# Kernel tuning notes

Hardware: AMD Instinct MI355X
Metric: run time of the kernel (lower is better)

Reference implementation:

```python
import jax, jax.numpy as jnp
from jax import lax
import numpy as np

N, L, C, G, K = 8, 4096, 256, 8, 3
GC = C // G
DILATION = 1
OFFSET_SCALE = 1.0
LN_EPS = 1e-6


def setup_inputs() -> dict:
    key = jax.random.key(0)
    ks = jax.random.split(key, 14)
    s = lambda k, shp, sc: jax.random.normal(k, shp, jnp.float32) * sc
    return {
        "x": jax.random.normal(ks[0], (N, L, C), jnp.float32),
        "W_in": s(ks[1], (C, C), (1.0 / C) ** 0.5),      # input_proj (in,out)
        "b_in": jnp.zeros((C,), jnp.float32),
        "conv_w": s(ks[2], (C, 1, K), 0.2),              # depthwise conv (O, I/g, K)
        "conv_b": jnp.zeros((C,), jnp.float32),
        "ln_g": jnp.ones((C,), jnp.float32),
        "ln_b": jnp.zeros((C,), jnp.float32),
        "W_off": s(ks[3], (C, G * K), 0.02),             # offset_linear
        "b_off": s(ks[4], (G * K,), 0.02),
        "W_mask": s(ks[5], (C, G * K), 0.02),            # mask_linear
        "b_mask": s(ks[6], (G * K,), 0.02),
        "W_out": s(ks[7], (C, C), (1.0 / C) ** 0.5),     # output_proj
        "b_out": jnp.zeros((C,), jnp.float32),
    }


def _dcnv3_1d(x, W_in, b_in, conv_w, conv_b, ln_g, ln_b,
              W_off, b_off, W_mask, b_mask, W_out, b_out):
    # x: (N, L, C)
    x_proj = x @ W_in + b_in                                     # (N,L,C)

    # depthwise conv -> LayerNorm(C) -> GELU  (the offset/mask feature branch)
    xc = x.transpose(0, 2, 1)                                    # (N,C,L)
    pad = (K - 1) // 2
    y = lax.conv_general_dilated(
        xc, conv_w, window_strides=(1,), padding=[(pad, pad)],
        dimension_numbers=("NCH", "OIH", "NCH"), feature_group_count=C)
    y = y + conv_b[None, :, None]
    y = y.transpose(0, 2, 1)                                     # (N,L,C)
    mu = y.mean(-1, keepdims=True)
    var = ((y - mu) ** 2).mean(-1, keepdims=True)
    y = (y - mu) * lax.rsqrt(var + LN_EPS) * ln_g + ln_b
    x_feat = jax.nn.gelu(y, approximate=False)                   # torch GELU = exact erf

    offset = (x_feat @ W_off + b_off).reshape(N, L, G, K)
    mask = jax.nn.softmax((x_feat @ W_mask + b_mask).reshape(N, L, G, K), axis=-1)

    # sampling locations (grid_sample with align_corners=True unnormalizes back to loc)
    ref_p = jnp.arange(L, dtype=jnp.float32)                     # (L,)
    lo = float(-((K - 1) // 2))
    hi = float((K - 1) // 2)
    dil_grid = jnp.linspace(lo, hi, K) * DILATION                # (K,)
    loc = ref_p[None, :, None, None] + dil_grid[None, None, None, :] \
          + offset * OFFSET_SCALE                                # (N,L,G,K)
    loc = jnp.remainder(loc, L)                                  # in [0, L)

    # bilinear sample along L with zero padding (matches F.grid_sample, H=1)
    f0 = jnp.floor(loc)
    w1 = loc - f0
    w0 = 1.0 - w1
    i0 = jnp.clip(f0.astype(jnp.int32), 0, L - 1)
    i1 = i0 + 1
    valid1 = (i1 < L)
    i1c = jnp.where(valid1, i1, 0)

    x_g = x_proj.reshape(N, L, G, GC)                            # (N,L,G,gc)
    nidx = jnp.arange(N)[:, None, None, None]
    gidx = jnp.arange(G)[None, None, :, None]
    v0 = x_g[nidx, i0, gidx]                                     # (N,L,G,K,gc)
    v1 = x_g[nidx, i1c, gidx] * valid1[..., None].astype(x_g.dtype)
    sampled = w0[..., None] * v0 + w1[..., None] * v1            # (N,L,G,K,gc)

    out = (sampled * mask[..., None]).sum(axis=3)                # (N,L,G,gc)
    out = out.reshape(N, L, C)
    return out @ W_out + b_out


def reference(x, W_in, b_in, conv_w, conv_b, ln_g, ln_b,
              W_off, b_off, W_mask, b_mask, W_out, b_out):
    return _dcnv3_1d(x, W_in, b_in, conv_w, conv_b, ln_g, ln_b,
                     W_off, b_off, W_mask, b_mask, W_out, b_out)
```

## Files before the change

### kernel.cpp

```cpp
#include <hip/hip_runtime.h>
#include <math.h>

constexpr int LL = 4096;
constexpr int CC = 256;
constexpr int MM = 32768;

typedef unsigned int u32;
typedef unsigned short u16;
typedef __attribute__((ext_vector_type(8))) short bf16x8;
typedef __attribute__((ext_vector_type(4))) float f32x4;

__device__ __forceinline__ u16 f2b(float f) {
    u32 u = __float_as_uint(f);
    u32 r = (u + 0x7fffu + ((u >> 16) & 1u)) >> 16;
    return (u16)r;
}
__device__ __forceinline__ u32 pack2(float a, float b) {
    return (u32)f2b(a) | ((u32)f2b(b) << 16);
}

__device__ __forceinline__ void gl_lds16(const u16* g, u16* l) {
    __builtin_amdgcn_global_load_lds(
        (const __attribute__((address_space(1))) unsigned int*)g,
        (__attribute__((address_space(3))) unsigned int*)l, 16, 0, 0);
}

__global__ __launch_bounds__(256) void conv_prep(
    const float* __restrict__ x, const float* __restrict__ cw,
    const float* __restrict__ cbias, const float* __restrict__ lng,
    const float* __restrict__ lnb, u16* __restrict__ xf,
    const float* __restrict__ W_in, const float* __restrict__ W_out,
    const float* __restrict__ W_off, const float* __restrict__ W_mask,
    u16* __restrict__ Wt_in, u16* __restrict__ Wt_out, u16* __restrict__ Wcomb)
{
    const int bid = blockIdx.x;
    const int t = threadIdx.x;
    if (bid >= 4096) {
        const int b = bid - 4096;
        if (b < 256) {
            Wt_in[b * 256 + t]  = f2b(W_in[t * 256 + b]);
            Wt_out[b * 256 + t] = f2b(W_out[t * 256 + b]);
        } else {
            const int j = b - 256;
            const float v = (j < 24) ? W_off[t * 24 + j] : W_mask[t * 24 + (j - 24)];
            Wcomb[j * 256 + t] = f2b(v);
        }
        return;
    }

    const int wave = t >> 6;
    const int lane = t & 63;
    const int nl0 = (bid << 3) + wave * 2;
    const int l0 = nl0 & (LL - 1);
    const int c0 = lane << 2;
    const size_t base = (size_t)nl0 * CC + c0;

    const float4 zero = make_float4(0.f, 0.f, 0.f, 0.f);
    float4 xm = (l0 > 0) ? *(const float4*)&x[base - CC] : zero;
    float4 xa = *(const float4*)&x[base];
    float4 xb = *(const float4*)&x[base + CC];
    float4 xp = (l0 < LL - 2) ? *(const float4*)&x[base + 2 * CC] : zero;

    const float cw0[4] = {cw[(c0+0)*3+0], cw[(c0+1)*3+0], cw[(c0+2)*3+0], cw[(c0+3)*3+0]};
    const float cw1[4] = {cw[(c0+0)*3+1], cw[(c0+1)*3+1], cw[(c0+2)*3+1], cw[(c0+3)*3+1]};
    const float cw2[4] = {cw[(c0+0)*3+2], cw[(c0+1)*3+2], cw[(c0+2)*3+2], cw[(c0+3)*3+2]};
    const float cb4[4] = {cbias[c0+0], cbias[c0+1], cbias[c0+2], cbias[c0+3]};
    const float lg4[4] = {lng[c0+0], lng[c0+1], lng[c0+2], lng[c0+3]};
    const float lb4[4] = {lnb[c0+0], lnb[c0+1], lnb[c0+2], lnb[c0+3]};

    const float pA[4] = {xm.x, xm.y, xm.z, xm.w};
    const float cA[4] = {xa.x, xa.y, xa.z, xa.w};
    const float nA[4] = {xb.x, xb.y, xb.z, xb.w};
    const float nB[4] = {xp.x, xp.y, xp.z, xp.w};

    float yA[4], yB[4];
    float sA = 0.f, qA = 0.f, sB = 0.f, qB = 0.f;
#pragma unroll
    for (int j = 0; j < 4; ++j) {
        float vA = fmaf(pA[j], cw0[j], fmaf(cA[j], cw1[j], fmaf(nA[j], cw2[j], cb4[j])));
        float vB = fmaf(cA[j], cw0[j], fmaf(nA[j], cw1[j], fmaf(nB[j], cw2[j], cb4[j])));
        yA[j] = vA; sA += vA; qA += vA * vA;
        yB[j] = vB; sB += vB; qB += vB * vB;
    }
#pragma unroll
    for (int off = 32; off > 0; off >>= 1) {
        sA += __shfl_xor(sA, off);
        qA += __shfl_xor(qA, off);
        sB += __shfl_xor(sB, off);
        qB += __shfl_xor(qB, off);
    }
    const float muA = sA * (1.f / CC), muB = sB * (1.f / CC);
    const float rsA = rsqrtf(qA * (1.f / CC) - muA * muA + 1e-6f);
    const float rsB = rsqrtf(qB * (1.f / CC) - muB * muB + 1e-6f);

    ushort4 oA, oB;
    float vA[4], vB[4];
#pragma unroll
    for (int j = 0; j < 4; ++j) {
        const float tA = (yA[j] - muA) * rsA * lg4[j] + lb4[j];
        const float tB = (yB[j] - muB) * rsB * lg4[j] + lb4[j];
        vA[j] = 0.5f * tA * (1.f + erff(tA * 0.70710678118654752f));
        vB[j] = 0.5f * tB * (1.f + erff(tB * 0.70710678118654752f));
    }
    oA.x = f2b(vA[0]); oA.y = f2b(vA[1]); oA.z = f2b(vA[2]); oA.w = f2b(vA[3]);
    oB.x = f2b(vB[0]); oB.y = f2b(vB[1]); oB.z = f2b(vB[2]); oB.w = f2b(vB[3]);
    *(ushort4*)&xf[base] = oA;
    *(ushort4*)&xf[base + CC] = oB;
}

__global__ __launch_bounds__(256) void proj_soft(
    const u16* __restrict__ xfeatb, const u16* __restrict__ Wcomb,
    const float* __restrict__ boff, const float* __restrict__ bmask,
    uint2* __restrict__ rec)
{
    __shared__ float logit[64 * 50];

    const int t = threadIdx.x;
    const int w = t >> 6, lane = t & 63;
    const int lr = lane & 15, lk8 = (lane >> 4) * 8;
    const int r0 = (lane >> 4) * 4;
    const int blk = blockIdx.x;
    const size_t row0 = (size_t)blk * 64;

    f32x4 pacc[3];
#pragma unroll
    for (int ct = 0; ct < 3; ++ct) pacc[ct] = f32x4{0.f, 0.f, 0.f, 0.f};
    const u16* fbase = xfeatb + (row0 + w * 16 + lr) * 256;
#pragma unroll
    for (int ks = 0; ks < 8; ++ks) {
        const int ke = ks * 32 + lk8;
        bf16x8 a = *(const bf16x8*)(fbase + ke);
#pragma unroll
        for (int ct = 0; ct < 3; ++ct) {
            bf16x8 bfr = *(const bf16x8*)(Wcomb + (size_t)(ct * 16 + lr) * 256 + ke);
            pacc[ct] = __builtin_amdgcn_mfma_f32_16x16x32_bf16(a, bfr, pacc[ct], 0, 0, 0);
        }
    }
#pragma unroll
    for (int ct = 0; ct < 3; ++ct) {
        const int j = ct * 16 + lr;
        const float bj = (j < 24) ? boff[j] : bmask[j - 24];
#pragma unroll
        for (int r4 = 0; r4 < 4; ++r4)
            logit[(w * 16 + r0 + r4) * 50 + j] = pacc[ct][r4] + bj;
    }
    __syncthreads();

#pragma unroll
    for (int pi = 0; pi < 2; ++pi) {
        const int pp = pi * 256 + t;
        const int rw = pp >> 3, g = pp & 7;
        const float* lp = &logit[rw * 50];
        const float m0v = lp[24 + g * 3 + 0];
        const float m1v = lp[24 + g * 3 + 1];
        const float m2v = lp[24 + g * 3 + 2];
        const float mx = fmaxf(m0v, fmaxf(m1v, m2v));
        const float e0 = expf(m0v - mx), e1 = expf(m1v - mx), e2 = expf(m2v - mx);
        const float inv = 1.f / (e0 + e1 + e2);
        const float msk[3] = {e0 * inv, e1 * inv, e2 * inv};
        const float lf = (float)((blk & 63) * 64 + rw);
        uint2* rbase = rec + row0 * 24 + pp * 3;
#pragma unroll
        for (int k = 0; k < 3; ++k) {
            const float loc = lf + (float)(k - 1) + lp[g * 3 + k];
            float r = fmodf(loc, (float)LL);
            if (r < 0.f) r += (float)LL;
            const float f0 = floorf(r);
            int i0 = (int)f0;
            i0 = i0 < 0 ? 0 : (i0 > LL - 1 ? LL - 1 : i0);
            const int i1 = i0 + 1;
            const float w1 = r - f0;
            const bool valid = (i1 < LL);
            union { u32 uw; _Float16 h[2]; } uh;
            uh.h[0] = (_Float16)(msk[k] * (1.f - w1));
            uh.h[1] = (_Float16)(valid ? msk[k] * w1 : 0.f);
            const u32 ij = (u32)i0 | ((u32)(valid ? i1 : 0) << 16);
            rbase[k] = make_uint2(uh.uw, ij);
        }
    }
}

__global__ __launch_bounds__(256, 2) void gemm1(
    const float* __restrict__ x, const u16* __restrict__ Wt_in,
    const float* __restrict__ b_in, u16* __restrict__ xprojb)
{
    __shared__ u16 As[2][128 * 32];
    __shared__ u16 Bs[2][128 * 32];

    const int t = threadIdx.x;
    const int w = t >> 6, lane = t & 63;
    const int lr = lane & 15, lk = lane >> 4;
    const int wm = w >> 1, wn = w & 1;

    const int d = blockIdx.x;
    const int m_t = (d & 7) * 32 + (d >> 4);
    const int n_t = (d >> 3) & 1;
    const int m0 = m_t * 128, n0 = n_t * 128;

    const int srow = lane >> 2;
    const int scol = (lane & 3) * 8;
    const int arow = t >> 1;
    const int akh = (t & 1) * 16;

    f32x4 acc[4][4];
#pragma unroll
    for (int i = 0; i < 4; ++i)
#pragma unroll
        for (int j = 0; j < 4; ++j) acc[i][j] = f32x4{0.f, 0.f, 0.f, 0.f};

    auto STAGE_B = [&](int buf, int kt) {
        const int k0 = kt * 32;
#pragma unroll
        for (int j = 0; j < 2; ++j) {
            const int rr = (w * 2 + j) * 16 + srow;
            gl_lds16(Wt_in + ((size_t)(n0 + rr) << 8) + k0 + scol,
                     &Bs[buf][0] + (w * 2 + j) * 512);
        }
    };
    const float* Abase = x + (size_t)(m0 + arow) * 256 + akh;

    {
        float4 f0 = *(const float4*)(Abase);
        float4 f1 = *(const float4*)(Abase + 4);
        float4 f2 = *(const float4*)(Abase + 8);
        float4 f3 = *(const float4*)(Abase + 12);
        STAGE_B(0, 0);
        u16* dst = &As[0][arow * 32 + akh];
        ((u32*)dst)[0] = pack2(f0.x, f0.y); ((u32*)dst)[1] = pack2(f0.z, f0.w);
        ((u32*)dst)[2] = pack2(f1.x, f1.y); ((u32*)dst)[3] = pack2(f1.z, f1.w);
        ((u32*)dst)[4] = pack2(f2.x, f2.y); ((u32*)dst)[5] = pack2(f2.z, f2.w);
        ((u32*)dst)[6] = pack2(f3.x, f3.y); ((u32*)dst)[7] = pack2(f3.z, f3.w);
    }

#pragma unroll
    for (int kt = 0; kt < 8; ++kt) {
        const int cur = kt & 1;
        __syncthreads();
        float4 f0, f1, f2, f3;
        if (kt < 7) {
            const float* ap = Abase + (kt + 1) * 32;
            f0 = *(const float4*)(ap);
            f1 = *(const float4*)(ap + 4);
            f2 = *(const float4*)(ap + 8);
            f3 = *(const float4*)(ap + 12);
            STAGE_B(cur ^ 1, kt + 1);
        }
        bf16x8 af[4], bfr[4];
#pragma unroll
        for (int mt = 0; mt < 4; ++mt)
            af[mt] = *(const bf16x8*)&As[cur][(wm * 64 + mt * 16 + lr) * 32 + lk * 8];
#pragma unroll
        for (int nt = 0; nt < 4; ++nt)
            bfr[nt] = *(const bf16x8*)&Bs[cur][(wn * 64 + nt * 16 + lr) * 32 + lk * 8];
#pragma unroll
        for (int mt = 0; mt < 4; ++mt)
#pragma unroll
            for (int nt = 0; nt < 4; ++nt)
                acc[mt][nt] = __builtin_amdgcn_mfma_f32_16x16x32_bf16(
                    af[mt], bfr[nt], acc[mt][nt], 0, 0, 0);
        if (kt < 7) {
            u16* dst = &As[cur ^ 1][arow * 32 + akh];
            ((u32*)dst)[0] = pack2(f0.x, f0.y); ((u32*)dst)[1] = pack2(f0.z, f0.w);
            ((u32*)dst)[2] = pack2(f1.x, f1.y); ((u32*)dst)[3] = pack2(f1.z, f1.w);
            ((u32*)dst)[4] = pack2(f2.x, f2.y); ((u32*)dst)[5] = pack2(f2.z, f2.w);
            ((u32*)dst)[6] = pack2(f3.x, f3.y); ((u32*)dst)[7] = pack2(f3.z, f3.w);
        }
    }

    const int r0 = lk * 4;
#pragma unroll
    for (int nt = 0; nt < 4; ++nt) {
        const int cn = n0 + wn * 64 + nt * 16 + lr;
        const float bv = b_in[cn];
#pragma unroll
        for (int mt = 0; mt < 4; ++mt)
#pragma unroll
            for (int r4 = 0; r4 < 4; ++r4)
                xprojb[(size_t)(m0 + wm * 64 + mt * 16 + r0 + r4) * 256 + cn] =
                    f2b(acc[mt][nt][r4] + bv);
    }
}

__global__ __launch_bounds__(256, 4) void gather_gemm(
    const uint2* __restrict__ rec, const u16* __restrict__ xprojb,
    const u16* __restrict__ Wt_out, const float* __restrict__ b_out,
    float* __restrict__ out)
{
    __shared__ __align__(16) char s_mem[16384];
    __shared__ uint2 s_pack[768];

    const int t = threadIdx.x;
    const int w = t >> 6, lane = t & 63;
    const int lr = lane & 15, lk8 = (lane >> 4) * 8;
    const int r0 = (lane >> 4) * 4;
    const int blk = blockIdx.x;
    const size_t row0 = (size_t)blk * 32;

    {
        const uint2* rb = rec + row0 * 24;
#pragma unroll
        for (int e = 0; e < 3; ++e) s_pack[t * 3 + e] = rb[t * 3 + e];
    }
    __syncthreads();

    {
        const int ig = t >> 5, tc = t & 31;
        const int c0 = tc * 8, g4 = tc >> 2;
        const u16* xpn = xprojb + (size_t)(blk >> 7) * LL * 256;
        const int ibeg = ig * 4;
#pragma unroll
        for (int i = ibeg; i < ibeg + 4; ++i) {
            const int bidx = (i * 8 + g4) * 3;
            float v[8] = {0.f, 0.f, 0.f, 0.f, 0.f, 0.f, 0.f, 0.f};
#pragma unroll
            for (int k = 0; k < 3; ++k) {
                const uint2 pk = s_pack[bidx + k];
                union { u32 uw; _Float16 h[2]; } uh; uh.uw = pk.x;
                const float wa = (float)uh.h[0], wb = (float)uh.h[1];
                const int i0 = (int)(pk.y & 0xffffu), i1 = (int)(pk.y >> 16);
                uint4 ua = *(const uint4*)(xpn + (size_t)i0 * 256 + c0);
                uint4 ub = *(const uint4*)(xpn + (size_t)i1 * 256 + c0);
                const u32 au[4] = {ua.x, ua.y, ua.z, ua.w};
                const u32 bu[4] = {ub.x, ub.y, ub.z, ub.w};
#pragma unroll
                for (int j = 0; j < 4; ++j) {
                    v[2 * j]     = fmaf(wa, __uint_as_float(au[j] << 16),
                                   fmaf(wb, __uint_as_float(bu[j] << 16), v[2 * j]));
                    v[2 * j + 1] = fmaf(wa, __uint_as_float(au[j] & 0xffff0000u),
                                   fmaf(wb, __uint_as_float(bu[j] & 0xffff0000u), v[2 * j + 1]));
                }
            }
            uint4 wd;
            wd.x = pack2(v[0], v[1]); wd.y = pack2(v[2], v[3]);
            wd.z = pack2(v[4], v[5]); wd.w = pack2(v[6], v[7]);
            const int addr = (i * 512 + tc * 16) ^ ((i & 7) << 4);
            *(uint4*)(s_mem + addr) = wd;
        }
    }
    __syncthreads();

    f32x4 acc[2][4];
#pragma unroll
    for (int i = 0; i < 2; ++i)
#pragma unroll
        for (int j = 0; j < 4; ++j) acc[i][j] = f32x4{0.f, 0.f, 0.f, 0.f};

    const u16* Bw = Wt_out + (size_t)(w * 64) * 256;
#pragma unroll
    for (int ks = 0; ks < 8; ++ks) {
        bf16x8 af[2], bfr[4];
#pragma unroll
        for (int mt = 0; mt < 2; ++mt) {
            const int rm = mt * 16 + lr;
            const int addr = (rm * 512 + ks * 64 + lk8 * 2) ^ ((rm & 7) << 4);
            af[mt] = *(const bf16x8*)(s_mem + addr);
        }
        const int ke = ks * 32 + lk8;
#pragma unroll
        for (int nt = 0; nt < 4; ++nt)
            bfr[nt] = *(const bf16x8*)(Bw + (size_t)(nt * 16 + lr) * 256 + ke);
#pragma unroll
        for (int mt = 0; mt < 2; ++mt)
#pragma unroll
            for (int nt = 0; nt < 4; ++nt)
                acc[mt][nt] = __builtin_amdgcn_mfma_f32_16x16x32_bf16(
                    af[mt], bfr[nt], acc[mt][nt], 0, 0, 0);
    }
#pragma unroll
    for (int nt = 0; nt < 4; ++nt) {
        const int cn = w * 64 + nt * 16 + lr;
        const float bv = b_out[cn];
#pragma unroll
        for (int mt = 0; mt < 2; ++mt)
#pragma unroll
            for (int r4 = 0; r4 < 4; ++r4)
                out[(row0 + mt * 16 + r0 + r4) * 256 + cn] = acc[mt][nt][r4] + bv;
    }
}

extern "C" void kernel_launch(void* const* d_in, const int* in_sizes, int n_in,
                              void* d_out, int out_size, void* d_ws, size_t ws_size,
                              hipStream_t stream)
{
    const float* x      = (const float*)d_in[0];
    const float* W_in   = (const float*)d_in[1];
    const float* b_in   = (const float*)d_in[2];
    const float* conv_w = (const float*)d_in[3];
    const float* conv_b = (const float*)d_in[4];
    const float* ln_g   = (const float*)d_in[5];
    const float* ln_b   = (const float*)d_in[6];
    const float* W_off  = (const float*)d_in[7];
    const float* b_off  = (const float*)d_in[8];
    const float* W_mask = (const float*)d_in[9];
    const float* b_mask = (const float*)d_in[10];
    const float* W_out  = (const float*)d_in[11];
    const float* b_out  = (const float*)d_in[12];

    u16* xfeatb = (u16*)d_ws;
    u16* xprojb = (u16*)((char*)d_ws + 16777216);
    char* wsb   = (char*)d_ws + 33554432;
    u16* Wt_in  = (u16*)(wsb);
    u16* Wt_out = (u16*)(wsb + 131072);
    u16* Wcombp = (u16*)(wsb + 262144);
    uint2* rec  = (uint2*)((char*)d_ws + 50331648);

    conv_prep<<<4096 + 304, 256, 0, stream>>>(x, conv_w, conv_b, ln_g, ln_b, xfeatb,
                                              W_in, W_out, W_off, W_mask,
                                              Wt_in, Wt_out, Wcombp);
    proj_soft<<<512, 256, 0, stream>>>(xfeatb, Wcombp, b_off, b_mask, rec);
    gemm1<<<512, 256, 0, stream>>>(x, Wt_in, b_in, xprojb);
    gather_gemm<<<1024, 256, 0, stream>>>(rec, xprojb, Wt_out, b_out, (float*)d_out);
}
```

Baseline: 72.34 us.

## Fuse depthwise conv/LayerNorm/GELU into offset-mask projection kernel via LDS

Splits the weight conversion into its own small kernel. It fuses the conv+LN+GELU feature computation into the offset/mask projection kernel, keeping the bf16 features in a swizzled LDS tile instead of writing and re-reading a 16 MB global buffer. This removes a global round trip of the features. In exchange, the fused kernel holds 32 KB+ of LDS and has only 512 blocks doing serial per-row LN work, which may lower occupancy and latency hiding.

```diff
diff --git a/kernel.cpp b/kernel.cpp
--- a/kernel.cpp
+++ b/kernel.cpp
@@ -25,124 +25,129 @@
         (__attribute__((address_space(3))) unsigned int*)l, 16, 0, 0);
 }
 
-__global__ __launch_bounds__(256) void conv_prep(
-    const float* __restrict__ x, const float* __restrict__ cw,
-    const float* __restrict__ cbias, const float* __restrict__ lng,
-    const float* __restrict__ lnb, u16* __restrict__ xf,
+__global__ __launch_bounds__(256) void prep_w(
     const float* __restrict__ W_in, const float* __restrict__ W_out,
     const float* __restrict__ W_off, const float* __restrict__ W_mask,
     u16* __restrict__ Wt_in, u16* __restrict__ Wt_out, u16* __restrict__ Wcomb)
 {
-    const int bid = blockIdx.x;
-    const int t = threadIdx.x;
-    if (bid >= 4096) {
-        const int b = bid - 4096;
-        if (b < 256) {
-            Wt_in[b * 256 + t]  = f2b(W_in[t * 256 + b]);
-            Wt_out[b * 256 + t] = f2b(W_out[t * 256 + b]);
-        } else {
-            const int j = b - 256;
-            const float v = (j < 24) ? W_off[t * 24 + j] : W_mask[t * 24 + (j - 24)];
-            Wcomb[j * 256 + t] = f2b(v);
-        }
-        return;
-    }
-
-    const int wave = t >> 6;
-    const int lane = t & 63;
-    const int nl0 = (bid << 3) + wave * 2;
-    const int l0 = nl0 & (LL - 1);
-    const int c0 = lane << 2;
-    const size_t base = (size_t)nl0 * CC + c0;
-
-    const float4 zero = make_float4(0.f, 0.f, 0.f, 0.f);
-    float4 xm = (l0 > 0) ? *(const float4*)&x[base - CC] : zero;
-    float4 xa = *(const float4*)&x[base];
-    float4 xb = *(const float4*)&x[base + CC];
-    float4 xp = (l0 < LL - 2) ? *(const float4*)&x[base + 2 * CC] : zero;
-
-    const float cw0[4] = {cw[(c0+0)*3+0], cw[(c0+1)*3+0], cw[(c0+2)*3+0], cw[(c0+3)*3+0]};
-    const float cw1[4] = {cw[(c0+0)*3+1], cw[(c0+1)*3+1], cw[(c0+2)*3+1], cw[(c0+3)*3+1]};
-    const float cw2[4] = {cw[(c0+0)*3+2], cw[(c0+1)*3+2], cw[(c0+2)*3+2], cw[(c0+3)*3+2]};
-    const float cb4[4] = {cbias[c0+0], cbias[c0+1], cbias[c0+2], cbias[c0+3]};
-    const float lg4[4] = {lng[c0+0], lng[c0+1], lng[c0+2], lng[c0+3]};
-    const float lb4[4] = {lnb[c0+0], lnb[c0+1], lnb[c0+2], lnb[c0+3]};
-
-    const float pA[4] = {xm.x, xm.y, xm.z, xm.w};
-    const float cA[4] = {xa.x, xa.y, xa.z, xa.w};
-    const float nA[4] = {xb.x, xb.y, xb.z, xb.w};
-    const float nB[4] = {xp.x, xp.y, xp.z, xp.w};
-
-    float yA[4], yB[4];
-    float sA = 0.f, qA = 0.f, sB = 0.f, qB = 0.f;
-#pragma unroll
-    for (int j = 0; j < 4; ++j) {
-        float vA = fmaf(pA[j], cw0[j], fmaf(cA[j], cw1[j], fmaf(nA[j], cw2[j], cb4[j])));
-        float vB = fmaf(cA[j], cw0[j], fmaf(nA[j], cw1[j], fmaf(nB[j], cw2[j], cb4[j])));
-        yA[j] = vA; sA += vA; qA += vA * vA;
-        yB[j] = vB; sB += vB; qB += vB * vB;
-    }
-#pragma unroll
-    for (int off = 32; off > 0; off >>= 1) {
-        sA += __shfl_xor(sA, off);
-        qA += __shfl_xor(qA, off);
-        sB += __shfl_xor(sB, off);
-        qB += __shfl_xor(qB, off);
-    }
-    const float muA = sA * (1.f / CC), muB = sB * (1.f / CC);
-    const float rsA = rsqrtf(qA * (1.f / CC) - muA * muA + 1e-6f);
-    const float rsB = rsqrtf(qB * (1.f / CC) - muB * muB + 1e-6f);
-
-    ushort4 oA, oB;
-    float vA[4], vB[4];
-#pragma unroll
-    for (int j = 0; j < 4; ++j) {
-        const float tA = (yA[j] - muA) * rsA * lg4[j] + lb4[j];
-        const float tB = (yB[j] - muB) * rsB * lg4[j] + lb4[j];
-        vA[j] = 0.5f * tA * (1.f + erff(tA * 0.70710678118654752f));
-        vB[j] = 0.5f * tB * (1.f + erff(tB * 0.70710678118654752f));
-    }
-    oA.x = f2b(vA[0]); oA.y = f2b(vA[1]); oA.z = f2b(vA[2]); oA.w = f2b(vA[3]);
-    oB.x = f2b(vB[0]); oB.y = f2b(vB[1]); oB.z = f2b(vB[2]); oB.w = f2b(vB[3]);
-    *(ushort4*)&xf[base] = oA;
-    *(ushort4*)&xf[base + CC] = oB;
-}
-
-__global__ __launch_bounds__(256) void proj_soft(
-    const u16* __restrict__ xfeatb, const u16* __restrict__ Wcomb,
+    const int b = blockIdx.x, t = threadIdx.x;
+    if (b < 256) {
+        Wt_in[b * 256 + t]  = f2b(W_in[t * 256 + b]);
+        Wt_out[b * 256 + t] = f2b(W_out[t * 256 + b]);
+    } else {
+        const int j = b - 256;
+        const float v = (j < 24) ? W_off[t * 24 + j] : W_mask[t * 24 + (j - 24)];
+        Wcomb[j * 256 + t] = f2b(v);
+    }
+}
+
+__global__ __launch_bounds__(256) void conv_feat_proj(
+    const float* __restrict__ x, const float* __restrict__ cw,
+    const float* __restrict__ cbias, const float* __restrict__ lng,
+    const float* __restrict__ lnb, const u16* __restrict__ Wcomb,
     const float* __restrict__ boff, const float* __restrict__ bmask,
     uint2* __restrict__ rec)
 {
+    __shared__ __align__(16) u16 feat[64 * 256];
     __shared__ float logit[64 * 50];
 
     const int t = threadIdx.x;
     const int w = t >> 6, lane = t & 63;
+    const int blk = blockIdx.x;
+    const size_t row0 = (size_t)blk * 64;
+    const int l0 = (blk & 63) * 64;
+
+    {
+        const int c0 = lane << 2;
+        const int rb = w * 16;
+        const int lw = l0 + rb;
+        const float* xb = x + (row0 + rb) * CC + c0;
+
+        const float cw0[4] = {cw[(c0+0)*3+0], cw[(c0+1)*3+0], cw[(c0+2)*3+0], cw[(c0+3)*3+0]};
+        const float cw1[4] = {cw[(c0+0)*3+1], cw[(c0+1)*3+1], cw[(c0+2)*3+1], cw[(c0+3)*3+1]};
+        const float cw2[4] = {cw[(c0+0)*3+2], cw[(c0+1)*3+2], cw[(c0+2)*3+2], cw[(c0+3)*3+2]};
+        const float cb4[4] = {cbias[c0+0], cbias[c0+1], cbias[c0+2], cbias[c0+3]};
+        const float lg4[4] = {lng[c0+0], lng[c0+1], lng[c0+2], lng[c0+3]};
+        const float lb4[4] = {lnb[c0+0], lnb[c0+1], lnb[c0+2], lnb[c0+3]};
+
+        const float4 zero = make_float4(0.f, 0.f, 0.f, 0.f);
+        float4 prev = (lw > 0) ? *(const float4*)(xb - CC) : zero;
+        float4 cur  = *(const float4*)(xb);
+
+#pragma unroll 2
+        for (int ii = 0; ii < 8; ++ii) {
+            float4 n1 = *(const float4*)(xb + (size_t)(2 * ii + 1) * CC);
+            float4 n2 = (lw + 2 * ii + 2 < LL)
+                        ? *(const float4*)(xb + (size_t)(2 * ii + 2) * CC) : zero;
+            const float pA[4] = {prev.x, prev.y, prev.z, prev.w};
+            const float cA[4] = {cur.x, cur.y, cur.z, cur.w};
+            const float nA[4] = {n1.x, n1.y, n1.z, n1.w};
+            const float nB[4] = {n2.x, n2.y, n2.z, n2.w};
+
+            float yA[4], yB[4];
+            float sA = 0.f, qA = 0.f, sB = 0.f, qB = 0.f;
+#pragma unroll
+            for (int j = 0; j < 4; ++j) {
+                float vA = fmaf(pA[j], cw0[j], fmaf(cA[j], cw1[j], fmaf(nA[j], cw2[j], cb4[j])));
+                float vB = fmaf(cA[j], cw0[j], fmaf(nA[j], cw1[j], fmaf(nB[j], cw2[j], cb4[j])));
+                yA[j] = vA; sA += vA; qA += vA * vA;
+                yB[j] = vB; sB += vB; qB += vB * vB;
+            }
+#pragma unroll
+            for (int off = 32; off > 0; off >>= 1) {
+                sA += __shfl_xor(sA, off);
+                qA += __shfl_xor(qA, off);
+                sB += __shfl_xor(sB, off);
+                qB += __shfl_xor(qB, off);
+            }
+            const float muA = sA * (1.f / CC), muB = sB * (1.f / CC);
+            const float rsA = rsqrtf(qA * (1.f / CC) - muA * muA + 1e-6f);
+            const float rsB = rsqrtf(qB * (1.f / CC) - muB * muB + 1e-6f);
+
+            float vA[4], vB[4];
+#pragma unroll
+            for (int j = 0; j < 4; ++j) {
+                const float tA = (yA[j] - muA) * rsA * lg4[j] + lb4[j];
+                const float tB = (yB[j] - muB) * rsB * lg4[j] + lb4[j];
+                vA[j] = 0.5f * tA * (1.f + erff(tA * 0.70710678118654752f));
+                vB[j] = 0.5f * tB * (1.f + erff(tB * 0.70710678118654752f));
+            }
+            const int rowA = rb + 2 * ii, rowB = rowA + 1;
+            const int adA = (rowA * 512 + c0 * 2) ^ ((rowA & 7) << 4);
+            const int adB = (rowB * 512 + c0 * 2) ^ ((rowB & 7) << 4);
+            *(uint2*)((char*)feat + adA) = make_uint2(pack2(vA[0], vA[1]), pack2(vA[2], vA[3]));
+            *(uint2*)((char*)feat + adB) = make_uint2(pack2(vB[0], vB[1]), pack2(vB[2], vB[3]));
+            prev = n1; cur = n2;
+        }
+    }
+
     const int lr = lane & 15, lk8 = (lane >> 4) * 8;
     const int r0 = (lane >> 4) * 4;
-    const int blk = blockIdx.x;
-    const size_t row0 = (size_t)blk * 64;
-
-    f32x4 pacc[3];
-#pragma unroll
-    for (int ct = 0; ct < 3; ++ct) pacc[ct] = f32x4{0.f, 0.f, 0.f, 0.f};
-    const u16* fbase = xfeatb + (row0 + w * 16 + lr) * 256;
-#pragma unroll
-    for (int ks = 0; ks < 8; ++ks) {
-        const int ke = ks * 32 + lk8;
-        bf16x8 a = *(const bf16x8*)(fbase + ke);
+    {
+        f32x4 pacc[3];
+#pragma unroll
+        for (int ct = 0; ct < 3; ++ct) pacc[ct] = f32x4{0.f, 0.f, 0.f, 0.f};
+        const int arow = w * 16 + lr;
+        const int abase = arow * 512;
+        const int amask = (arow & 7) << 4;
+#pragma unroll
+        for (int ks = 0; ks < 8; ++ks) {
+            const int ke = ks * 32 + lk8;
+            bf16x8 a = *(const bf16x8*)((const char*)feat + ((abase + ke * 2) ^ amask));
+#pragma unroll
+            for (int ct = 0; ct < 3; ++ct) {
+                bf16x8 bfr = *(const bf16x8*)(Wcomb + (size_t)(ct * 16 + lr) * 256 + ke);
+                pacc[ct] = __builtin_amdgcn_mfma_f32_16x16x32_bf16(a, bfr, pacc[ct], 0, 0, 0);
+            }
+        }
 #pragma unroll
         for (int ct = 0; ct < 3; ++ct) {
-            bf16x8 bfr = *(const bf16x8*)(Wcomb + (size_t)(ct * 16 + lr) * 256 + ke);
-            pacc[ct] = __builtin_amdgcn_mfma_f32_16x16x32_bf16(a, bfr, pacc[ct], 0, 0, 0);
-        }
-    }
-#pragma unroll
-    for (int ct = 0; ct < 3; ++ct) {
-        const int j = ct * 16 + lr;
-        const float bj = (j < 24) ? boff[j] : bmask[j - 24];
-#pragma unroll
-        for (int r4 = 0; r4 < 4; ++r4)
-            logit[(w * 16 + r0 + r4) * 50 + j] = pacc[ct][r4] + bj;
+            const int j = ct * 16 + lr;
+            const float bj = (j < 24) ? boff[j] : bmask[j - 24];
+#pragma unroll
+            for (int r4 = 0; r4 < 4; ++r4)
+                logit[(w * 16 + r0 + r4) * 50 + j] = pacc[ct][r4] + bj;
+        }
     }
     __syncthreads();
 
@@ -158,7 +163,7 @@
         const float e0 = expf(m0v - mx), e1 = expf(m1v - mx), e2 = expf(m2v - mx);
         const float inv = 1.f / (e0 + e1 + e2);
         const float msk[3] = {e0 * inv, e1 * inv, e2 * inv};
-        const float lf = (float)((blk & 63) * 64 + rw);
+        const float lf = (float)(l0 + rw);
         uint2* rbase = rec + row0 * 24 + pp * 3;
 #pragma unroll
         for (int k = 0; k < 3; ++k) {
@@ -396,7 +401,6 @@
     const float* W_out  = (const float*)d_in[11];
     const float* b_out  = (const float*)d_in[12];
 
-    u16* xfeatb = (u16*)d_ws;
     u16* xprojb = (u16*)((char*)d_ws + 16777216);
     char* wsb   = (char*)d_ws + 33554432;
     u16* Wt_in  = (u16*)(wsb);
@@ -404,10 +408,9 @@
     u16* Wcombp = (u16*)(wsb + 262144);
     uint2* rec  = (uint2*)((char*)d_ws + 50331648);
 
-    conv_prep<<<4096 + 304, 256, 0, stream>>>(x, conv_w, conv_b, ln_g, ln_b, xfeatb,
-                                              W_in, W_out, W_off, W_mask,
-                                              Wt_in, Wt_out, Wcombp);
-    proj_soft<<<512, 256, 0, stream>>>(xfeatb, Wcombp, b_off, b_mask, rec);
+    prep_w<<<304, 256, 0, stream>>>(W_in, W_out, W_off, W_mask, Wt_in, Wt_out, Wcombp);
+    conv_feat_proj<<<512, 256, 0, stream>>>(x, conv_w, conv_b, ln_g, ln_b,
+                                            Wcombp, b_off, b_mask, rec);
     gemm1<<<512, 256, 0, stream>>>(x, Wt_in, b_in, xprojb);
     gather_gemm<<<1024, 256, 0, stream>>>(rec, xprojb, Wt_out, b_out, (float*)d_out);
 }
```

Result: no change. 73.48 us (+1.6%).
